# Kernel tuning notes

Measured on AMD Instinct MI355X. Metric: run time of the kernel, lower is better.

Reference implementation:

```python
import jax, jax.numpy as jnp
import numpy as np

N = 100000
E = 1000000
NODE_DIM = 128
EDGE_DIM = 32
HID = 64
HIER = 32
NUM_CLASS = 10
NUM_LAYERS = 3
BN_EPS = 1e-5


def setup_inputs() -> dict:
    key = jax.random.key(0)
    ks = jax.random.split(key, 16)
    s = 0.05
    return {
        "x": jax.random.normal(ks[0], (N, NODE_DIM), jnp.float32),
        "e": jax.random.normal(ks[1], (E, EDGE_DIM), jnp.float32),
        "c": jax.random.normal(ks[2], (N, HIER), jnp.float32),
        "w_node": jax.random.normal(ks[3], (NODE_DIM, HID), jnp.float32) * s,
        "b_node": jnp.zeros((HID,), jnp.float32),
        "w_edge": jax.random.normal(ks[4], (EDGE_DIM, HID), jnp.float32) * s,
        "b_edge": jnp.zeros((HID,), jnp.float32),
        "w_out1": jax.random.normal(ks[5], (HIER + HID, 2 * HID), jnp.float32) * s,
        "b_out1": jnp.zeros((2 * HID,), jnp.float32),
        "bn_gamma": jnp.ones((2 * HID,), jnp.float32),
        "bn_beta": jnp.zeros((2 * HID,), jnp.float32),
        "prelu_a": jnp.asarray(0.25, jnp.float32),
        "w_out2": jax.random.normal(ks[6], (2 * HID, NUM_CLASS), jnp.float32) * s,
        "b_out2": jnp.zeros((NUM_CLASS,), jnp.float32),
        "edge_index": jax.random.randint(ks[7], (2, E), 0, N, jnp.int64),
    }


def reference(x, e, c, w_node, b_node, w_edge, b_edge, w_out1, b_out1,
              bn_gamma, bn_beta, prelu_a, w_out2, b_out2, edge_index):
    n = x.shape[0]
    h = x @ w_node + b_node                      # [N, HID]
    eh = e @ w_edge + b_edge                     # [E, HID]
    src, dst = edge_index[0], edge_index[1]
    loop = jnp.arange(n)
    # add_self_loops + zero self-loop edge_attr (done inside each GCN layer,
    # identical every layer so hoisted)
    src_f = jnp.concatenate([src, loop])
    dst_f = jnp.concatenate([dst, loop])
    e_f = jnp.concatenate([eh, jnp.zeros((n, eh.shape[1]), eh.dtype)], axis=0)
    deg = jax.ops.segment_sum(jnp.ones(dst_f.shape, x.dtype), dst_f, num_segments=n)
    dinv = deg ** -0.5                           # deg >= 1 thanks to self loops
    norm = (dinv[src_f] * dinv[dst_f])[:, None]  # [E+N, 1]
    h_sum = h
    for _ in range(NUM_LAYERS):
        msg = norm * (h[src_f] + e_f)            # gather + edge compute
        h = jax.ops.segment_sum(msg, dst_f, num_segments=n)  # scatter-add
        h = jax.nn.leaky_relu(h, 0.2)
        h_sum = h_sum + h                        # sum over h_list
    z = jnp.concatenate([h_sum, c], axis=-1) @ w_out1 + b_out1
    # BatchNorm1d (training-mode batch statistics, biased variance)
    mu = z.mean(axis=0)
    var = z.var(axis=0)
    z = (z - mu) / jnp.sqrt(var + BN_EPS) * bn_gamma + bn_beta
    z = jnp.where(z > 0, z, prelu_a * z)         # PReLU (single param)
    return z @ w_out2 + b_out2
```

## Files before the change

kernel.cpp:

```cpp
#include <hip/hip_runtime.h>
#include <math.h>

#define N_NODES 100000
#define N_EDGES 1000000
#define HID     64
#define HIER    32
#define NDIM    128
#define EDIM    32
#define K1      96
#define C1      128
#define NCLS    10
#define BN_EPS  1e-5f
#define SCAN_B  98
#define ZTILES  782
#define HTILES2 782

__device__ __forceinline__ unsigned pk_bf16(float a, float b) {
    unsigned ua = __float_as_uint(a);
    ua = (ua + 0x7FFFu + ((ua >> 16) & 1u)) >> 16;
    unsigned ub = __float_as_uint(b);
    ub = (ub + 0x7FFFu + ((ub >> 16) & 1u)) & 0xFFFF0000u;
    return ua | ub;
}
__device__ __forceinline__ float bf_lo(unsigned g) { return __uint_as_float(g << 16); }
__device__ __forceinline__ float bf_hi(unsigned g) { return __uint_as_float(g & 0xFFFF0000u); }


__global__ void k_count(const int* __restrict__ ei, int* __restrict__ cnt) {
    int i = blockIdx.x * blockDim.x + threadIdx.x;
    if (i < N_EDGES) atomicAdd(&cnt[ei[N_EDGES + i]], 1);
}

__global__ void k_scan1(const int* __restrict__ cnt, int* __restrict__ offs,
                        float* __restrict__ dinv, int* __restrict__ bsum) {
    __shared__ int buf[2][1024];
    int t = threadIdx.x, b = blockIdx.x;
    int i = b * 1024 + t;
    int v = (i < N_NODES) ? cnt[i] : 0;
    buf[0][t] = v; __syncthreads();
    int pi = 0;
    for (int off = 1; off < 1024; off <<= 1) {
        int x = buf[pi][t];
        if (t >= off) x += buf[pi][t - off];
        buf[pi ^ 1][t] = x; __syncthreads(); pi ^= 1;
    }
    int incl = buf[pi][t];
    if (i < N_NODES) {
        offs[i] = incl - v;
        dinv[i] = rsqrtf((float)(v + 1));
    }
    if (t == 1023) bsum[b] = incl;
}

__global__ void k_scan2(int* __restrict__ bsum, int nb) {
    __shared__ int buf[2][1024];
    int t = threadIdx.x;
    int v = (t < nb) ? bsum[t] : 0;
    buf[0][t] = v; __syncthreads();
    int pi = 0;
    for (int off = 1; off < 1024; off <<= 1) {
        int x = buf[pi][t];
        if (t >= off) x += buf[pi][t - off];
        buf[pi ^ 1][t] = x; __syncthreads(); pi ^= 1;
    }
    int incl = buf[pi][t];
    if (t < nb) bsum[t] = incl - v;
}

__global__ void k_scan3(const int* __restrict__ bsum, int* __restrict__ offs) {
    int b = blockIdx.x;
    int i = b * 1024 + threadIdx.x;
    if (i < N_NODES) offs[i] += bsum[b];
    if (i == 0) offs[N_NODES] = N_EDGES;
}

__global__ void k_fill(const int* __restrict__ ei, const int* __restrict__ offs,
                       int* __restrict__ cursor, const float* __restrict__ dinv,
                       int4* __restrict__ epk) {
    int i = blockIdx.x * blockDim.x + threadIdx.x;
    if (i >= N_EDGES) return;
    int s = ei[i], d = ei[N_EDGES + i];
    int pos = offs[d] + atomicAdd(&cursor[d], 1);
    epk[pos] = make_int4(s, i, __float_as_int(dinv[s]), 0);
}


__global__ __launch_bounds__(256) void k_conv(const float4* __restrict__ e4,
                                              uint4* __restrict__ eb4) {
    int i = blockIdx.x * 256 + threadIdx.x;
    float4 a = e4[(size_t)2 * i];
    float4 b = e4[(size_t)2 * i + 1];
    uint4 pk;
    pk.x = pk_bf16(a.x, a.y); pk.y = pk_bf16(a.z, a.w);
    pk.z = pk_bf16(b.x, b.y); pk.w = pk_bf16(b.z, b.w);
    eb4[i] = pk;
}


__global__ __launch_bounds__(256) void k_agg3(const unsigned* __restrict__ ebfu,
                                              const int4* __restrict__ epk,
                                              const int* __restrict__ offs,
                                              const float* __restrict__ dinv,
                                              float* __restrict__ agg,
                                              float* __restrict__ wsumv) {
    int v = (blockIdx.x * 256 + threadIdx.x) >> 4;
    if (v >= N_NODES) return;
    int q = threadIdx.x & 15;
    int start = offs[v], end = offs[v + 1];
    float ax = 0.f, ay = 0.f, wacc = 0.f;
    for (int i = start; i < end; i += 4) {
        int i1 = i + 1, i2 = i + 2, i3 = i + 3;
        int4 p0 = epk[i];
        int4 p1 = (i1 < end) ? epk[i1] : make_int4(0, 0, 0, 0);
        int4 p2 = (i2 < end) ? epk[i2] : make_int4(0, 0, 0, 0);
        int4 p3 = (i3 < end) ? epk[i3] : make_int4(0, 0, 0, 0);
        float n0 = __int_as_float(p0.z), n1 = __int_as_float(p1.z);
        float n2 = __int_as_float(p2.z), n3 = __int_as_float(p3.z);
        unsigned g0 = ebfu[(size_t)p0.y * 16 + q];
        unsigned g1 = ebfu[(size_t)p1.y * 16 + q];
        unsigned g2 = ebfu[(size_t)p2.y * 16 + q];
        unsigned g3 = ebfu[(size_t)p3.y * 16 + q];
        ax += n0 * bf_lo(g0) + n1 * bf_lo(g1) + n2 * bf_lo(g2) + n3 * bf_lo(g3);
        ay += n0 * bf_hi(g0) + n1 * bf_hi(g1) + n2 * bf_hi(g2) + n3 * bf_hi(g3);
        wacc += n0 + n1 + n2 + n3;
    }
    float dv = dinv[v];
    *(float2*)&agg[(size_t)v * EDIM + q * 2] = make_float2(dv * ax, dv * ay);
    if (q == 0) wsumv[v] = dv * wacc;
}


__global__ __launch_bounds__(256) void k_h0t2(const float* __restrict__ x,
                                              const float* __restrict__ w,
                                              const float* __restrict__ bias,
                                              unsigned* __restrict__ hbf) {
    __shared__ unsigned wpk[NDIM * 36];
    __shared__ float xt[128 * 33];
    for (int i = threadIdx.x; i < NDIM * 32; i += 256) {
        int k = i >> 5, j = i & 31;
        wpk[k * 36 + j] = pk_bf16(w[k * HID + 2 * j], w[k * HID + 2 * j + 1]);
    }
    int tid = threadIdx.x;
    int lane = tid & 63, wave = tid >> 6;
    int lr = lane >> 3, lc = lane & 7;
    int rbase = wave * 32 + lr * 4;
    int cbase = lc * 8;
    float bA[8];
    #pragma unroll
    for (int j = 0; j < 8; ++j) bA[j] = bias[cbase + j];
    for (int tile = blockIdx.x; tile < HTILES2; tile += gridDim.x) {
        int row0 = tile * 128;
        float acc[4][8];
        #pragma unroll
        for (int i = 0; i < 4; ++i)
            #pragma unroll
            for (int j = 0; j < 8; ++j) acc[i][j] = 0.f;
        for (int ch = 0; ch < 4; ++ch) {
            __syncthreads();
            #pragma unroll
            for (int p = 0; p < 4; ++p) {
                int idx = p * 256 + tid;
                int row = idx >> 3, kq = idx & 7;
                int gk = ch * 32 + kq * 4;
                float4 v = make_float4(0.f, 0.f, 0.f, 0.f);
                int gr = row0 + row;
                if (gr < N_NODES) v = *(const float4*)&x[(size_t)gr * NDIM + gk];
                float* d = &xt[row * 33 + kq * 4];
                d[0] = v.x; d[1] = v.y; d[2] = v.z; d[3] = v.w;
            }
            __syncthreads();
            for (int k = 0; k < 32; ++k) {
                float u[4];
                #pragma unroll
                for (int i = 0; i < 4; ++i) u[i] = xt[(rbase + i) * 33 + k];
                uint4 wp = *(const uint4*)&wpk[(ch * 32 + k) * 36 + lc * 4];
                float wv[8];
                wv[0] = bf_lo(wp.x); wv[1] = bf_hi(wp.x);
                wv[2] = bf_lo(wp.y); wv[3] = bf_hi(wp.y);
                wv[4] = bf_lo(wp.z); wv[5] = bf_hi(wp.z);
                wv[6] = bf_lo(wp.w); wv[7] = bf_hi(wp.w);
                #pragma unroll
                for (int i = 0; i < 4; ++i)
                    #pragma unroll
                    for (int j = 0; j < 8; ++j) acc[i][j] += u[i] * wv[j];
            }
        }
        #pragma unroll
        for (int i = 0; i < 4; ++i) {
            int gr = row0 + rbase + i;
            if (gr < N_NODES) {
                uint4 pk;
                pk.x = pk_bf16(acc[i][0] + bA[0], acc[i][1] + bA[1]);
                pk.y = pk_bf16(acc[i][2] + bA[2], acc[i][3] + bA[3]);
                pk.z = pk_bf16(acc[i][4] + bA[4], acc[i][5] + bA[5]);
                pk.w = pk_bf16(acc[i][6] + bA[6], acc[i][7] + bA[7]);
                *(uint4*)&hbf[(size_t)gr * 32 + (cbase >> 1)] = pk;
            }
        }
    }
}


__global__ __launch_bounds__(256) void k_se(const float* __restrict__ agg,
                                            const float* __restrict__ wsumv,
                                            const float* __restrict__ we,
                                            const float* __restrict__ be,
                                            unsigned* __restrict__ sebf) {
    int lane = threadIdx.x & 63, wid = threadIdx.x >> 6;
    float wreg[EDIM];
    #pragma unroll
    for (int k = 0; k < EDIM; ++k) wreg[k] = we[k * HID + lane];
    float bl = be[lane];
    for (int v = blockIdx.x * 4 + wid; v < N_NODES; v += gridDim.x * 4) {
        const float4* ar = (const float4*)(agg + (size_t)v * EDIM);
        float acc = wsumv[v] * bl;
        #pragma unroll
        for (int k4 = 0; k4 < EDIM / 4; ++k4) {
            float4 av = ar[k4];
            int k = k4 * 4;
            acc += av.x * wreg[k + 0] + av.y * wreg[k + 1] +
                   av.z * wreg[k + 2] + av.w * wreg[k + 3];
        }
        float partner = __shfl_xor(acc, 1);
        if ((lane & 1) == 0)
            sebf[(size_t)v * 32 + (lane >> 1)] = pk_bf16(acc, partner);
    }
}


__global__ __launch_bounds__(256) void k_layer(const unsigned* __restrict__ hold,
                                               const unsigned* __restrict__ sebf,
                                               const int4* __restrict__ epk,
                                               const int* __restrict__ offs,
                                               const float* __restrict__ dinv,
                                               unsigned* __restrict__ hnew) {
    int gw = (blockIdx.x * 256 + threadIdx.x) >> 6;
    int lane = threadIdx.x & 63;
    int half = lane >> 5, dp = lane & 31;
    int v = gw * 2 + half;
    if (v >= N_NODES) return;
    int start = offs[v], end = offs[v + 1];
    float dv = dinv[v];
    size_t vp = (size_t)v * 32 + dp;
    unsigned hv = hold[vp];
    float a0 = dv * bf_lo(hv), a1 = dv * bf_hi(hv);
    for (int i = start; i < end; i += 8) {
        int idx[8]; float nn[8]; unsigned gg[8];
        #pragma unroll
        for (int u = 0; u < 8; ++u) {
            int ii = i + u;
            int4 p = (ii < end) ? epk[ii] : make_int4(0, 0, 0, 0);
            idx[u] = p.x;
            nn[u]  = __int_as_float(p.z);
        }
        #pragma unroll
        for (int u = 0; u < 8; ++u) gg[u] = hold[(size_t)idx[u] * 32 + dp];
        #pragma unroll
        for (int u = 0; u < 8; ++u) {
            a0 += nn[u] * bf_lo(gg[u]);
            a1 += nn[u] * bf_hi(gg[u]);
        }
    }
    unsigned sv = sebf[vp];
    float r0 = bf_lo(sv) + dv * a0;
    float r1 = bf_hi(sv) + dv * a1;
    r0 = (r0 > 0.f) ? r0 : 0.2f * r0;
    r1 = (r1 > 0.f) ? r1 : 0.2f * r1;
    hnew[vp] = pk_bf16(r0, r1);
}


__global__ __launch_bounds__(256) void k_zstats(const unsigned* __restrict__ hb0,
                                                const unsigned* __restrict__ hb1,
                                                const unsigned* __restrict__ hb2,
                                                const unsigned* __restrict__ hb3,
                                                const float* __restrict__ cfeat,
                                                const float* __restrict__ w1,
                                                const float* __restrict__ b1,
                                                unsigned* __restrict__ zbf,
                                                float* __restrict__ stats) {
    __shared__ unsigned wpk[K1 * 68];
    __shared__ float ut[128 * 49];
    __shared__ float red[4][64];
    for (int i = threadIdx.x; i < K1 * 64; i += 256) {
        int k = i >> 6, j = i & 63;
        wpk[k * 68 + j] = pk_bf16(w1[k * C1 + 2 * j], w1[k * C1 + 2 * j + 1]);
    }
    int tid = threadIdx.x;
    int lane = tid & 63, wave = tid >> 6;
    int lr = lane >> 3, lc = lane & 7;
    int wr = wave >> 1, wc = wave & 1;
    int rbase = wr * 64 + lr * 8;
    int cbase = wc * 64 + lc * 8;
    float bA[8];
    #pragma unroll
    for (int j = 0; j < 8; ++j) bA[j] = b1[cbase + j];
    float s[8], q[8];
    #pragma unroll
    for (int j = 0; j < 8; ++j) { s[j] = 0.f; q[j] = 0.f; }

    for (int tile = blockIdx.x; tile < ZTILES; tile += gridDim.x) {
        int row0 = tile * 128;
        float acc[8][8];
        #pragma unroll
        for (int i = 0; i < 8; ++i)
            #pragma unroll
            for (int j = 0; j < 8; ++j) acc[i][j] = 0.f;
        for (int ch = 0; ch < 2; ++ch) {
            int kbase = ch * 48;
            __syncthreads();
            #pragma unroll
            for (int p = 0; p < 6; ++p) {
                int idx = p * 256 + tid;
                int row = idx / 12, kq = idx % 12;
                int gk = kbase + kq * 4;
                int gr = row0 + row;
                float f0 = 0.f, f1 = 0.f, f2 = 0.f, f3 = 0.f;
                if (gr < N_NODES) {
                    if (gk < HID) {
                        size_t o = (size_t)gr * 32 + (gk >> 1);
                        uint2 g0 = *(const uint2*)&hb0[o];
                        uint2 g1 = *(const uint2*)&hb1[o];
                        uint2 g2 = *(const uint2*)&hb2[o];
                        uint2 g3 = *(const uint2*)&hb3[o];
                        f0 = bf_lo(g0.x) + bf_lo(g1.x) + bf_lo(g2.x) + bf_lo(g3.x);
                        f1 = bf_hi(g0.x) + bf_hi(g1.x) + bf_hi(g2.x) + bf_hi(g3.x);
                        f2 = bf_lo(g0.y) + bf_lo(g1.y) + bf_lo(g2.y) + bf_lo(g3.y);
                        f3 = bf_hi(g0.y) + bf_hi(g1.y) + bf_hi(g2.y) + bf_hi(g3.y);
                    } else {
                        float4 v = *(const float4*)&cfeat[(size_t)gr * HIER + (gk - HID)];
                        f0 = v.x; f1 = v.y; f2 = v.z; f3 = v.w;
                    }
                }
                float* d = &ut[row * 49 + kq * 4];
                d[0] = f0; d[1] = f1; d[2] = f2; d[3] = f3;
            }
            __syncthreads();
            for (int k = 0; k < 48; ++k) {
                float u[8];
                #pragma unroll
                for (int i = 0; i < 8; ++i) u[i] = ut[(rbase + i) * 49 + k];
                uint4 wp = *(const uint4*)&wpk[(kbase + k) * 68 + (cbase >> 1)];
                float wv[8];
                wv[0] = bf_lo(wp.x); wv[1] = bf_hi(wp.x);
                wv[2] = bf_lo(wp.y); wv[3] = bf_hi(wp.y);
                wv[4] = bf_lo(wp.z); wv[5] = bf_hi(wp.z);
                wv[6] = bf_lo(wp.w); wv[7] = bf_hi(wp.w);
                #pragma unroll
                for (int i = 0; i < 8; ++i) {
                    acc[i][0] += u[i] * wv[0]; acc[i][1] += u[i] * wv[1];
                    acc[i][2] += u[i] * wv[2]; acc[i][3] += u[i] * wv[3];
                    acc[i][4] += u[i] * wv[4]; acc[i][5] += u[i] * wv[5];
                    acc[i][6] += u[i] * wv[6]; acc[i][7] += u[i] * wv[7];
                }
            }
        }
        #pragma unroll
        for (int i = 0; i < 8; ++i) {
            int gr = row0 + rbase + i;
            if (gr < N_NODES) {
                float zz[8];
                #pragma unroll
                for (int j = 0; j < 8; ++j) {
                    zz[j] = acc[i][j] + bA[j];
                    s[j] += zz[j]; q[j] += zz[j] * zz[j];
                }
                uint4 pk;
                pk.x = pk_bf16(zz[0], zz[1]); pk.y = pk_bf16(zz[2], zz[3]);
                pk.z = pk_bf16(zz[4], zz[5]); pk.w = pk_bf16(zz[6], zz[7]);
                *(uint4*)&zbf[(size_t)gr * 64 + (cbase >> 1)] = pk;
            }
        }
    }

    #pragma unroll
    for (int j = 0; j < 8; ++j) {
        s[j] += __shfl_xor(s[j], 8); s[j] += __shfl_xor(s[j], 16); s[j] += __shfl_xor(s[j], 32);
        q[j] += __shfl_xor(q[j], 8); q[j] += __shfl_xor(q[j], 16); q[j] += __shfl_xor(q[j], 32);
    }
    __syncthreads();
    if (lr == 0) {
        #pragma unroll
        for (int j = 0; j < 8; ++j) red[wave][lc * 8 + j] = s[j];
    }
    __syncthreads();
    if (tid < 128) {
        int wc2 = tid >> 6, cl = tid & 63;
        atomicAdd(&stats[wc2 * 64 + cl], red[wc2][cl] + red[wc2 + 2][cl]);
    }
    __syncthreads();
    if (lr == 0) {
        #pragma unroll
        for (int j = 0; j < 8; ++j) red[wave][lc * 8 + j] = q[j];
    }
    __syncthreads();
    if (tid < 128) {
        int wc2 = tid >> 6, cl = tid & 63;
        atomicAdd(&stats[C1 + wc2 * 64 + cl], red[wc2][cl] + red[wc2 + 2][cl]);
    }
}

__global__ void k_ab(const float* __restrict__ stats, const float* __restrict__ gamma,
                     const float* __restrict__ beta, float* __restrict__ ab) {
    int t = threadIdx.x;
    if (t < C1) {
        float mu = stats[t] / (float)N_NODES;
        float var = stats[C1 + t] / (float)N_NODES - mu * mu;
        float inv = rsqrtf(var + BN_EPS);
        float a = gamma[t] * inv;
        ab[t] = a;
        ab[C1 + t] = beta[t] - mu * a;
    }
}


__global__ __launch_bounds__(256) void k_out3(const unsigned* __restrict__ zbf,
                                              const float* __restrict__ ab,
                                              const float* __restrict__ pa,
                                              const float* __restrict__ w2,
                                              const float* __restrict__ b2,
                                              float* __restrict__ out) {
    int v = blockIdx.x * 256 + threadIdx.x;
    if (v >= N_NODES) return;
    float alpha = pa[0];
    float acc[NCLS];
    #pragma unroll
    for (int j = 0; j < NCLS; ++j) acc[j] = b2[j];
    const uint4* zr = (const uint4*)(zbf + (size_t)v * 64);
    #pragma unroll
    for (int pk4 = 0; pk4 < 16; ++pk4) {
        uint4 g = zr[pk4];
        unsigned gw[4] = {g.x, g.y, g.z, g.w};
        #pragma unroll
        for (int w = 0; w < 4; ++w) {
            int d0 = pk4 * 8 + w * 2;
            float p0 = bf_lo(gw[w]) * ab[d0]     + ab[C1 + d0];
            float p1 = bf_hi(gw[w]) * ab[d0 + 1] + ab[C1 + d0 + 1];
            p0 = (p0 > 0.f) ? p0 : alpha * p0;
            p1 = (p1 > 0.f) ? p1 : alpha * p1;
            #pragma unroll
            for (int j = 0; j < NCLS; ++j)
                acc[j] += p0 * w2[d0 * NCLS + j] + p1 * w2[(d0 + 1) * NCLS + j];
        }
    }
    #pragma unroll
    for (int j = 0; j < NCLS; ++j) out[(size_t)v * NCLS + j] = acc[j];
}


extern "C" void kernel_launch(void* const* d_in, const int* in_sizes, int n_in,
                              void* d_out, int out_size, void* d_ws, size_t ws_size,
                              hipStream_t stream) {
    const float* x      = (const float*)d_in[0];
    const float* e      = (const float*)d_in[1];
    const float* c      = (const float*)d_in[2];
    const float* w_node = (const float*)d_in[3];
    const float* b_node = (const float*)d_in[4];
    const float* w_edge = (const float*)d_in[5];
    const float* b_edge = (const float*)d_in[6];
    const float* w_out1 = (const float*)d_in[7];
    const float* b_out1 = (const float*)d_in[8];
    const float* gamma  = (const float*)d_in[9];
    const float* beta   = (const float*)d_in[10];
    const float* pa     = (const float*)d_in[11];
    const float* w_out2 = (const float*)d_in[12];
    const float* b_out2 = (const float*)d_in[13];
    const int*   ei     = (const int*)d_in[14];
    float* out = (float*)d_out;

    char* wsb = (char*)d_ws;
    ushort*   ebf  = (ushort*)wsb;
    unsigned* sebf = (unsigned*)wsb;
    unsigned* zbf  = (unsigned*)(wsb + 12800000);
    size_t off = (64000000 + 255) & ~(size_t)255;
    auto alloc = [&](size_t bytes) {
        void* p = wsb + off;
        off = (off + bytes + 255) & ~(size_t)255;
        return p;
    };
    int*      cnt      = (int*)alloc(4ull * N_NODES);
    int*      offs     = (int*)alloc(4ull * (N_NODES + 1));
    float*    dinv     = (float*)alloc(4ull * N_NODES);
    int*      bsum     = (int*)alloc(4ull * 128);
    int4*     epk      = (int4*)alloc(16ull * N_EDGES);
    float*    agg      = (float*)alloc(4ull * N_NODES * EDIM);
    float*    wsumv    = (float*)alloc(4ull * N_NODES);
    float*    stats    = (float*)alloc(4ull * 256);
    float*    ab       = (float*)alloc(4ull * 256);
    unsigned* hb0      = (unsigned*)alloc(4ull * N_NODES * 32);
    unsigned* hb1      = (unsigned*)alloc(4ull * N_NODES * 32);
    unsigned* hb2      = (unsigned*)alloc(4ull * N_NODES * 32);
    unsigned* hb3      = (unsigned*)alloc(4ull * N_NODES * 32);

    hipMemsetAsync(cnt, 0, 4ull * N_NODES, stream);
    hipMemsetAsync(stats, 0, 4ull * 256, stream);

    k_count<<<(N_EDGES + 255) / 256, 256, 0, stream>>>(ei, cnt);
    k_scan1<<<SCAN_B, 1024, 0, stream>>>(cnt, offs, dinv, bsum);
    k_scan2<<<1, 1024, 0, stream>>>(bsum, SCAN_B);
    k_scan3<<<SCAN_B, 1024, 0, stream>>>(bsum, offs);
    hipMemsetAsync(cnt, 0, 4ull * N_NODES, stream);
    k_fill<<<(N_EDGES + 255) / 256, 256, 0, stream>>>(ei, offs, cnt, dinv, epk);

    k_conv<<<15625, 256, 0, stream>>>((const float4*)e, (uint4*)ebf);
    k_agg3<<<N_NODES * 16 / 256, 256, 0, stream>>>((const unsigned*)ebf, epk,
                                                   offs, dinv, agg, wsumv);

    k_se<<<1280, 256, 0, stream>>>(agg, wsumv, w_edge, b_edge, sebf);
    k_h0t2<<<HTILES2, 256, 0, stream>>>(x, w_node, b_node, hb0);

    k_layer<<<N_NODES / 8, 256, 0, stream>>>(hb0, sebf, epk, offs, dinv, hb1);
    k_layer<<<N_NODES / 8, 256, 0, stream>>>(hb1, sebf, epk, offs, dinv, hb2);
    k_layer<<<N_NODES / 8, 256, 0, stream>>>(hb2, sebf, epk, offs, dinv, hb3);

    k_zstats<<<ZTILES, 256, 0, stream>>>(hb0, hb1, hb2, hb3, c, w_out1, b_out1, zbf, stats);
    k_ab<<<1, 128, 0, stream>>>(stats, gamma, beta, ab);
    k_out3<<<(N_NODES + 255) / 256, 256, 0, stream>>>(zbf, ab, pa, w_out2, b_out2, out);
}
```

Baseline: 455.1 us.

## Widen layer gathers, fuse h-sum into last layer, bf16 transposed zstats staging

The GCN layer kernel now uses 16 lanes per node, each gathering 8-byte uint2 chunks instead of 4-byte words, which halves the lanes per node and widens the loads. The final layer also computes the running sum h0+h1+h2+h3 and writes it as bf16, so the z-stats kernel reads one packed sum buffer instead of four h buffers. The c features are pre-converted to bf16 by a new small kernel. The z-stats kernel stages its whole K=96 tile once as a transposed packed-bf16 layout with vectorized LDS reads, dropping the two-chunk loop. The trade-off is an extra conversion kernel and bf16 rounding of the summed features and of c.

```diff
diff --git a/kernel.cpp b/kernel.cpp
--- a/kernel.cpp
+++ b/kernel.cpp
@@ -94,6 +94,14 @@
     pk.x = pk_bf16(a.x, a.y); pk.y = pk_bf16(a.z, a.w);
     pk.z = pk_bf16(b.x, b.y); pk.w = pk_bf16(b.z, b.w);
     eb4[i] = pk;
+}
+
+__global__ __launch_bounds__(256) void k_conv2(const float4* __restrict__ c4,
+                                               uint2* __restrict__ cb2) {
+    int i = blockIdx.x * 256 + threadIdx.x;
+    if (i >= N_NODES * 8) return;
+    float4 a = c4[i];
+    cb2[i] = make_uint2(pk_bf16(a.x, a.y), pk_bf16(a.z, a.w));
 }
 
 
@@ -134,7 +142,7 @@
                                               const float* __restrict__ w,
                                               const float* __restrict__ bias,
                                               unsigned* __restrict__ hbf) {
-    __shared__ unsigned wpk[NDIM * 36];
+    __shared__ __align__(16) unsigned wpk[NDIM * 36];
     __shared__ float xt[128 * 33];
     for (int i = threadIdx.x; i < NDIM * 32; i += 256) {
         int k = i >> 5, j = i & 31;
@@ -228,24 +236,23 @@
 }
 
 
-__global__ __launch_bounds__(256) void k_layer(const unsigned* __restrict__ hold,
-                                               const unsigned* __restrict__ sebf,
-                                               const int4* __restrict__ epk,
-                                               const int* __restrict__ offs,
-                                               const float* __restrict__ dinv,
-                                               unsigned* __restrict__ hnew) {
-    int gw = (blockIdx.x * 256 + threadIdx.x) >> 6;
-    int lane = threadIdx.x & 63;
-    int half = lane >> 5, dp = lane & 31;
-    int v = gw * 2 + half;
+__global__ __launch_bounds__(256) void k_layer4(const unsigned* __restrict__ hold,
+                                                const unsigned* __restrict__ sebf,
+                                                const int4* __restrict__ epk,
+                                                const int* __restrict__ offs,
+                                                const float* __restrict__ dinv,
+                                                unsigned* __restrict__ hnew) {
+    int v = (blockIdx.x * 256 + threadIdx.x) >> 4;
     if (v >= N_NODES) return;
+    int q = threadIdx.x & 15;
     int start = offs[v], end = offs[v + 1];
     float dv = dinv[v];
-    size_t vp = (size_t)v * 32 + dp;
-    unsigned hv = hold[vp];
-    float a0 = dv * bf_lo(hv), a1 = dv * bf_hi(hv);
+    size_t vp = (size_t)v * 16 + q;
+    uint2 hv = ((const uint2*)hold)[vp];
+    float a0 = dv * bf_lo(hv.x), a1 = dv * bf_hi(hv.x);
+    float a2 = dv * bf_lo(hv.y), a3 = dv * bf_hi(hv.y);
     for (int i = start; i < end; i += 8) {
-        int idx[8]; float nn[8]; unsigned gg[8];
+        int idx[8]; float nn[8]; uint2 gg[8];
         #pragma unroll
         for (int u = 0; u < 8; ++u) {
             int ii = i + u;
@@ -254,33 +261,88 @@
             nn[u]  = __int_as_float(p.z);
         }
         #pragma unroll
-        for (int u = 0; u < 8; ++u) gg[u] = hold[(size_t)idx[u] * 32 + dp];
+        for (int u = 0; u < 8; ++u) gg[u] = ((const uint2*)hold)[(size_t)idx[u] * 16 + q];
         #pragma unroll
         for (int u = 0; u < 8; ++u) {
-            a0 += nn[u] * bf_lo(gg[u]);
-            a1 += nn[u] * bf_hi(gg[u]);
-        }
-    }
-    unsigned sv = sebf[vp];
-    float r0 = bf_lo(sv) + dv * a0;
-    float r1 = bf_hi(sv) + dv * a1;
+            a0 += nn[u] * bf_lo(gg[u].x); a1 += nn[u] * bf_hi(gg[u].x);
+            a2 += nn[u] * bf_lo(gg[u].y); a3 += nn[u] * bf_hi(gg[u].y);
+        }
+    }
+    uint2 sv = ((const uint2*)sebf)[vp];
+    float r0 = bf_lo(sv.x) + dv * a0;
+    float r1 = bf_hi(sv.x) + dv * a1;
+    float r2 = bf_lo(sv.y) + dv * a2;
+    float r3 = bf_hi(sv.y) + dv * a3;
     r0 = (r0 > 0.f) ? r0 : 0.2f * r0;
     r1 = (r1 > 0.f) ? r1 : 0.2f * r1;
-    hnew[vp] = pk_bf16(r0, r1);
-}
-
-
-__global__ __launch_bounds__(256) void k_zstats(const unsigned* __restrict__ hb0,
-                                                const unsigned* __restrict__ hb1,
-                                                const unsigned* __restrict__ hb2,
-                                                const unsigned* __restrict__ hb3,
-                                                const float* __restrict__ cfeat,
+    r2 = (r2 > 0.f) ? r2 : 0.2f * r2;
+    r3 = (r3 > 0.f) ? r3 : 0.2f * r3;
+    ((uint2*)hnew)[vp] = make_uint2(pk_bf16(r0, r1), pk_bf16(r2, r3));
+}
+
+__global__ __launch_bounds__(256) void k_layer4s(const unsigned* __restrict__ hold,
+                                                 const unsigned* __restrict__ hb0,
+                                                 const unsigned* __restrict__ hb1,
+                                                 const unsigned* __restrict__ sebf,
+                                                 const int4* __restrict__ epk,
+                                                 const int* __restrict__ offs,
+                                                 const float* __restrict__ dinv,
+                                                 unsigned* __restrict__ hnew,
+                                                 unsigned* __restrict__ hsbf) {
+    int v = (blockIdx.x * 256 + threadIdx.x) >> 4;
+    if (v >= N_NODES) return;
+    int q = threadIdx.x & 15;
+    int start = offs[v], end = offs[v + 1];
+    float dv = dinv[v];
+    size_t vp = (size_t)v * 16 + q;
+    uint2 hv = ((const uint2*)hold)[vp];
+    float a0 = dv * bf_lo(hv.x), a1 = dv * bf_hi(hv.x);
+    float a2 = dv * bf_lo(hv.y), a3 = dv * bf_hi(hv.y);
+    for (int i = start; i < end; i += 8) {
+        int idx[8]; float nn[8]; uint2 gg[8];
+        #pragma unroll
+        for (int u = 0; u < 8; ++u) {
+            int ii = i + u;
+            int4 p = (ii < end) ? epk[ii] : make_int4(0, 0, 0, 0);
+            idx[u] = p.x;
+            nn[u]  = __int_as_float(p.z);
+        }
+        #pragma unroll
+        for (int u = 0; u < 8; ++u) gg[u] = ((const uint2*)hold)[(size_t)idx[u] * 16 + q];
+        #pragma unroll
+        for (int u = 0; u < 8; ++u) {
+            a0 += nn[u] * bf_lo(gg[u].x); a1 += nn[u] * bf_hi(gg[u].x);
+            a2 += nn[u] * bf_lo(gg[u].y); a3 += nn[u] * bf_hi(gg[u].y);
+        }
+    }
+    uint2 sv = ((const uint2*)sebf)[vp];
+    float r0 = bf_lo(sv.x) + dv * a0;
+    float r1 = bf_hi(sv.x) + dv * a1;
+    float r2 = bf_lo(sv.y) + dv * a2;
+    float r3 = bf_hi(sv.y) + dv * a3;
+    r0 = (r0 > 0.f) ? r0 : 0.2f * r0;
+    r1 = (r1 > 0.f) ? r1 : 0.2f * r1;
+    r2 = (r2 > 0.f) ? r2 : 0.2f * r2;
+    r3 = (r3 > 0.f) ? r3 : 0.2f * r3;
+    ((uint2*)hnew)[vp] = make_uint2(pk_bf16(r0, r1), pk_bf16(r2, r3));
+    uint2 g0 = ((const uint2*)hb0)[vp];
+    uint2 g1 = ((const uint2*)hb1)[vp];
+    float s0 = r0 + bf_lo(g0.x) + bf_lo(g1.x) + bf_lo(hv.x);
+    float s1 = r1 + bf_hi(g0.x) + bf_hi(g1.x) + bf_hi(hv.x);
+    float s2 = r2 + bf_lo(g0.y) + bf_lo(g1.y) + bf_lo(hv.y);
+    float s3 = r3 + bf_hi(g0.y) + bf_hi(g1.y) + bf_hi(hv.y);
+    ((uint2*)hsbf)[vp] = make_uint2(pk_bf16(s0, s1), pk_bf16(s2, s3));
+}
+
+
+__global__ __launch_bounds__(256) void k_zstats(const unsigned* __restrict__ hsbf,
+                                                const unsigned* __restrict__ cbf,
                                                 const float* __restrict__ w1,
                                                 const float* __restrict__ b1,
                                                 unsigned* __restrict__ zbf,
                                                 float* __restrict__ stats) {
-    __shared__ unsigned wpk[K1 * 68];
-    __shared__ float ut[128 * 49];
+    __shared__ __align__(16) unsigned wpk[K1 * 68];
+    __shared__ __align__(16) unsigned ut[K1 * 68];
     __shared__ float red[4][64];
     for (int i = threadIdx.x; i < K1 * 64; i += 256) {
         int k = i >> 6, j = i & 63;
@@ -292,6 +354,8 @@
     int wr = wave >> 1, wc = wave & 1;
     int rbase = wr * 64 + lr * 8;
     int cbase = wc * 64 + lc * 8;
+    int kslot = wave;
+    int rp = lane;
     float bA[8];
     #pragma unroll
     for (int j = 0; j < 8; ++j) bA[j] = b1[cbase + j];
@@ -301,58 +365,50 @@
 
     for (int tile = blockIdx.x; tile < ZTILES; tile += gridDim.x) {
         int row0 = tile * 128;
+        __syncthreads();
+        {
+            int r0g = row0 + 2 * rp, r1g = r0g + 1;
+            bool ok0 = r0g < N_NODES, ok1 = r1g < N_NODES;
+            #pragma unroll
+            for (int kku = 0; kku < 12; ++kku) {
+                int ku = kslot * 12 + kku;
+                unsigned A = 0u, B = 0u;
+                if (ku < 32) {
+                    if (ok0) A = hsbf[(size_t)r0g * 32 + ku];
+                    if (ok1) B = hsbf[(size_t)r1g * 32 + ku];
+                } else {
+                    if (ok0) A = cbf[(size_t)r0g * 16 + (ku - 32)];
+                    if (ok1) B = cbf[(size_t)r1g * 16 + (ku - 32)];
+                }
+                int k0 = 2 * ku;
+                ut[k0 * 68 + rp]       = (A & 0xFFFFu) | (B << 16);
+                ut[(k0 + 1) * 68 + rp] = (A >> 16) | (B & 0xFFFF0000u);
+            }
+        }
+        __syncthreads();
         float acc[8][8];
         #pragma unroll
         for (int i = 0; i < 8; ++i)
             #pragma unroll
             for (int j = 0; j < 8; ++j) acc[i][j] = 0.f;
-        for (int ch = 0; ch < 2; ++ch) {
-            int kbase = ch * 48;
-            __syncthreads();
+        for (int k = 0; k < K1; ++k) {
+            uint4 up = *(const uint4*)&ut[k * 68 + wr * 32 + lr * 4];
+            uint4 wp = *(const uint4*)&wpk[k * 68 + wc * 32 + lc * 4];
+            float u[8], wv[8];
+            u[0] = bf_lo(up.x); u[1] = bf_hi(up.x);
+            u[2] = bf_lo(up.y); u[3] = bf_hi(up.y);
+            u[4] = bf_lo(up.z); u[5] = bf_hi(up.z);
+            u[6] = bf_lo(up.w); u[7] = bf_hi(up.w);
+            wv[0] = bf_lo(wp.x); wv[1] = bf_hi(wp.x);
+            wv[2] = bf_lo(wp.y); wv[3] = bf_hi(wp.y);
+            wv[4] = bf_lo(wp.z); wv[5] = bf_hi(wp.z);
+            wv[6] = bf_lo(wp.w); wv[7] = bf_hi(wp.w);
             #pragma unroll
-            for (int p = 0; p < 6; ++p) {
-                int idx = p * 256 + tid;
-                int row = idx / 12, kq = idx % 12;
-                int gk = kbase + kq * 4;
-                int gr = row0 + row;
-                float f0 = 0.f, f1 = 0.f, f2 = 0.f, f3 = 0.f;
-                if (gr < N_NODES) {
-                    if (gk < HID) {
-                        size_t o = (size_t)gr * 32 + (gk >> 1);
-                        uint2 g0 = *(const uint2*)&hb0[o];
-                        uint2 g1 = *(const uint2*)&hb1[o];
-                        uint2 g2 = *(const uint2*)&hb2[o];
-                        uint2 g3 = *(const uint2*)&hb3[o];
-                        f0 = bf_lo(g0.x) + bf_lo(g1.x) + bf_lo(g2.x) + bf_lo(g3.x);
-                        f1 = bf_hi(g0.x) + bf_hi(g1.x) + bf_hi(g2.x) + bf_hi(g3.x);
-                        f2 = bf_lo(g0.y) + bf_lo(g1.y) + bf_lo(g2.y) + bf_lo(g3.y);
-                        f3 = bf_hi(g0.y) + bf_hi(g1.y) + bf_hi(g2.y) + bf_hi(g3.y);
-                    } else {
-                        float4 v = *(const float4*)&cfeat[(size_t)gr * HIER + (gk - HID)];
-                        f0 = v.x; f1 = v.y; f2 = v.z; f3 = v.w;
-                    }
-                }
-                float* d = &ut[row * 49 + kq * 4];
-                d[0] = f0; d[1] = f1; d[2] = f2; d[3] = f3;
-            }
-            __syncthreads();
-            for (int k = 0; k < 48; ++k) {
-                float u[8];
-                #pragma unroll
-                for (int i = 0; i < 8; ++i) u[i] = ut[(rbase + i) * 49 + k];
-                uint4 wp = *(const uint4*)&wpk[(kbase + k) * 68 + (cbase >> 1)];
-                float wv[8];
-                wv[0] = bf_lo(wp.x); wv[1] = bf_hi(wp.x);
-                wv[2] = bf_lo(wp.y); wv[3] = bf_hi(wp.y);
-                wv[4] = bf_lo(wp.z); wv[5] = bf_hi(wp.z);
-                wv[6] = bf_lo(wp.w); wv[7] = bf_hi(wp.w);
-                #pragma unroll
-                for (int i = 0; i < 8; ++i) {
-                    acc[i][0] += u[i] * wv[0]; acc[i][1] += u[i] * wv[1];
-                    acc[i][2] += u[i] * wv[2]; acc[i][3] += u[i] * wv[3];
-                    acc[i][4] += u[i] * wv[4]; acc[i][5] += u[i] * wv[5];
-                    acc[i][6] += u[i] * wv[6]; acc[i][7] += u[i] * wv[7];
-                }
+            for (int i = 0; i < 8; ++i) {
+                acc[i][0] += u[i] * wv[0]; acc[i][1] += u[i] * wv[1];
+                acc[i][2] += u[i] * wv[2]; acc[i][3] += u[i] * wv[3];
+                acc[i][4] += u[i] * wv[4]; acc[i][5] += u[i] * wv[5];
+                acc[i][6] += u[i] * wv[6]; acc[i][7] += u[i] * wv[7];
             }
         }
         #pragma unroll
@@ -491,6 +547,8 @@
     unsigned* hb1      = (unsigned*)alloc(4ull * N_NODES * 32);
     unsigned* hb2      = (unsigned*)alloc(4ull * N_NODES * 32);
     unsigned* hb3      = (unsigned*)alloc(4ull * N_NODES * 32);
+    unsigned* cbf      = (unsigned*)alloc(4ull * N_NODES * 16);
+    unsigned* hsbf     = (unsigned*)agg;
 
     hipMemsetAsync(cnt, 0, 4ull * N_NODES, stream);
     hipMemsetAsync(stats, 0, 4ull * 256, stream);
@@ -507,13 +565,15 @@
                                                    offs, dinv, agg, wsumv);
 
     k_se<<<1280, 256, 0, stream>>>(agg, wsumv, w_edge, b_edge, sebf);
+    k_conv2<<<(N_NODES * 8 + 255) / 256, 256, 0, stream>>>((const float4*)c, (uint2*)cbf);
     k_h0t2<<<HTILES2, 256, 0, stream>>>(x, w_node, b_node, hb0);
 
-    k_layer<<<N_NODES / 8, 256, 0, stream>>>(hb0, sebf, epk, offs, dinv, hb1);
-    k_layer<<<N_NODES / 8, 256, 0, stream>>>(hb1, sebf, epk, offs, dinv, hb2);
-    k_layer<<<N_NODES / 8, 256, 0, stream>>>(hb2, sebf, epk, offs, dinv, hb3);
-
-    k_zstats<<<ZTILES, 256, 0, stream>>>(hb0, hb1, hb2, hb3, c, w_out1, b_out1, zbf, stats);
+    k_layer4<<<N_NODES * 16 / 256, 256, 0, stream>>>(hb0, sebf, epk, offs, dinv, hb1);
+    k_layer4<<<N_NODES * 16 / 256, 256, 0, stream>>>(hb1, sebf, epk, offs, dinv, hb2);
+    k_layer4s<<<N_NODES * 16 / 256, 256, 0, stream>>>(hb2, hb0, hb1, sebf, epk, offs,
+                                                      dinv, hb3, hsbf);
+
+    k_zstats<<<ZTILES, 256, 0, stream>>>(hsbf, cbf, w_out1, b_out1, zbf, stats);
     k_ab<<<1, 128, 0, stream>>>(stats, gamma, beta, ab);
     k_out3<<<(N_NODES + 255) / 256, 256, 0, stream>>>(zbf, ab, pa, w_out2, b_out2, out);
 }
```

Result: faster. 435.0 us (-4.4%).
